# Performance work log

Hardware: AMD Instinct MI355X
Metric: run time of the kernel (lower is better)

The kernel has to match this reference:

```python
import jax, jax.numpy as jnp
import numpy as np

N = 5000      # batch entities / prompts
M = 50000     # flattened neighbors
R = 500000    # flattened (neighbor, relation) pairs
D = 768
VOCAB = 10000


def setup_inputs() -> dict:
    key = jax.random.key(0)
    ks = jax.random.split(key, 12)
    start_emb = jax.random.normal(ks[0], (N, D), dtype=jnp.float32)
    prompt_emb = jax.random.normal(ks[1], (N, D), dtype=jnp.float32)
    relation_emb = jax.random.normal(ks[2], (R, D), dtype=jnp.float32)
    neighbor_emb = jax.random.normal(ks[3], (M, D), dtype=jnp.float32)
    count_table = jax.random.normal(ks[4], (VOCAB, D), dtype=jnp.float32) * 0.02
    W = jax.random.normal(ks[5], (1, 4 * D), dtype=jnp.float32) * 0.02
    b = jnp.zeros((1,), dtype=jnp.float32)
    counts = jax.random.randint(ks[6], (R,), 0, VOCAB)
    rel_start_idx = jax.random.randint(ks[7], (R,), 0, N)
    neighbor_idx = jnp.sort(jax.random.randint(ks[8], (R,), 0, M))
    start_idx = jax.random.randint(ks[9], (M,), 0, N)
    return {
        "start_emb": start_emb, "prompt_emb": prompt_emb,
        "relation_emb": relation_emb, "neighbor_emb": neighbor_emb,
        "count_table": count_table, "W": W, "b": b,
        "counts": counts, "rel_start_idx": rel_start_idx,
        "neighbor_idx": neighbor_idx, "start_idx": start_idx,
    }


def _segment_softmax(logits, seg, num_segments):
    # numerically stable softmax within each neighbor segment
    seg_max = jax.ops.segment_max(logits, seg, num_segments=num_segments)
    ex = jnp.exp(logits - seg_max[seg])
    denom = jax.ops.segment_sum(ex, seg, num_segments=num_segments)
    return ex / denom[seg]


def reference(start_emb, prompt_emb, relation_emb, neighbor_emb,
              count_table, W, b,
              counts, rel_start_idx, neighbor_idx, start_idx):
    num_neighbors = neighbor_emb.shape[0]
    # relation_emb = relation_emb * count_embs(counts)   [R, D]
    rel = relation_emb * count_table[counts]
    # per-relation logit: <start_emb[rel_start_idx], rel>  [R]
    s_rel = start_emb[rel_start_idx]
    logits = jnp.sum(s_rel * rel, axis=1)
    # scatter_softmax over neighbor segments, then scatter_add aggregation
    alpha = _segment_softmax(logits, neighbor_idx, num_neighbors)
    rel_agg = jax.ops.segment_sum(rel * alpha[:, None], neighbor_idx,
                                  num_segments=num_neighbors)  # [M, D]
    # gather per-neighbor start / prompt embeddings
    s_n = start_emb[start_idx]      # [M, D]
    p_n = prompt_emb[start_idx]     # [M, D]
    # AttentionScorer: concat then Linear(4D -> 1), squeeze
    combined = jnp.concatenate([s_n, p_n, rel_agg, neighbor_emb], axis=1)
    score = (combined @ W.T + b).squeeze(-1)  # [M]
    return score
```

## Files before the change

kernel.cpp:

```cpp
#include <hip/hip_runtime.h>
#include <math.h>

#define WAVE 64

__device__ inline float wave_reduce_sum(float v) {
    #pragma unroll
    for (int off = 32; off > 0; off >>= 1)
        v += __shfl_xor(v, off, WAVE);
    return v;
}

__device__ inline unsigned int f32_to_e4m3(float a) {
    unsigned int u = __float_as_uint(a);
    unsigned int sgn = (u >> 31) << 7;
    unsigned int absu = u & 0x7FFFFFFFu;
    if (absu < 0x3C800000u) return sgn;
    int exp = (int)(absu >> 23) - 127;
    unsigned int m = absu & 0x7FFFFFu;
    unsigned int keep = m >> 20;
    unsigned int rest = m & 0xFFFFFu;
    if (rest > 0x80000u || (rest == 0x80000u && (keep & 1u))) keep++;
    if (keep == 8u) { keep = 0u; exp += 1; }
    if (exp > 8) { exp = 8; keep = 7u; }
    return sgn | ((unsigned int)(exp + 7) << 3) | keep;
}

__device__ inline float e4m3_to_f32(unsigned int b) {
    unsigned int expm = b & 0x7Fu;
    unsigned int f = ((b & 0x80u) << 24) | ((expm + (120u << 3)) << 20);
    float v = __uint_as_float(f);
    return (expm & 0x78u) ? v : 0.0f;
}

__device__ inline void decode4_fp8(unsigned int u, float& a, float& b, float& c, float& d) {
#if __has_builtin(__builtin_amdgcn_cvt_pk_f32_fp8)
    auto lo = __builtin_amdgcn_cvt_pk_f32_fp8(u, false);
    auto hi = __builtin_amdgcn_cvt_pk_f32_fp8(u, true);
    a = lo[0]; b = lo[1]; c = hi[0]; d = hi[1];
#else
    a = e4m3_to_f32(u & 0xFFu);
    b = e4m3_to_f32((u >> 8) & 0xFFu);
    c = e4m3_to_f32((u >> 16) & 0xFFu);
    d = e4m3_to_f32((u >> 24) & 0xFFu);
#endif
}

__global__ void cvt_fp8_kernel(const float* __restrict__ in,
                               unsigned int* __restrict__ out,
                               int n4, float scale) {
    int i = blockIdx.x * blockDim.x + threadIdx.x;
    if (i >= n4) return;
    float4 v = ((const float4*)in)[i];
    unsigned int b0 = f32_to_e4m3(v.x * scale);
    unsigned int b1 = f32_to_e4m3(v.y * scale);
    unsigned int b2 = f32_to_e4m3(v.z * scale);
    unsigned int b3 = f32_to_e4m3(v.w * scale);
    out[i] = b0 | (b1 << 8) | (b2 << 16) | (b3 << 24);
}

__global__ void entity_dots_kernel(const float* __restrict__ start_emb,
                                   const float* __restrict__ prompt_emb,
                                   const float* __restrict__ W,
                                   float* __restrict__ ew, int N, int D) {
    int wavesPerBlock = blockDim.x >> 6;
    int i = blockIdx.x * wavesPerBlock + (threadIdx.x >> 6);
    int lane = threadIdx.x & 63;
    if (i >= N) return;
    const float* s  = start_emb  + (size_t)i * D;
    const float* p  = prompt_emb + (size_t)i * D;
    const float* w0 = W;
    const float* w1 = W + D;
    float acc = 0.f;
    for (int idx = lane * 4; idx < D; idx += WAVE * 4) {
        float4 sv  = *(const float4*)(s  + idx);
        float4 pv  = *(const float4*)(p  + idx);
        float4 w0v = *(const float4*)(w0 + idx);
        float4 w1v = *(const float4*)(w1 + idx);
        acc = fmaf(sv.x, w0v.x, acc);
        acc = fmaf(sv.y, w0v.y, acc);
        acc = fmaf(sv.z, w0v.z, acc);
        acc = fmaf(sv.w, w0v.w, acc);
        acc = fmaf(pv.x, w1v.x, acc);
        acc = fmaf(pv.y, w1v.y, acc);
        acc = fmaf(pv.z, w1v.z, acc);
        acc = fmaf(pv.w, w1v.w, acc);
    }
    acc = wave_reduce_sum(acc);
    if (lane == 0) ew[i] = acc;
}

template <int DD>
__global__ __launch_bounds__(256) void relation_kernel2_t(
        const float* __restrict__ relation_emb,
        const unsigned char* __restrict__ ctf8,
        const unsigned char* __restrict__ sf8,
        const float* __restrict__ W,
        const int* __restrict__ counts,
        const int* __restrict__ rel_start_idx,
        float2* __restrict__ lt,
        int R, float inv_ct_scale) {
    int w = blockIdx.x * (blockDim.x >> 6) + (threadIdx.x >> 6);
    int lane = threadIdx.x & 63;
    int r0 = w << 1;
    if (r0 >= R) return;
    bool has2 = (r0 + 1 < R);

    int cnt0 = counts[r0];
    int st0  = rel_start_idx[r0];
    int cnt1 = has2 ? counts[r0 + 1] : cnt0;
    int st1  = has2 ? rel_start_idx[r0 + 1] : st0;

    const float* re0 = relation_emb + (size_t)r0 * DD;
    const float* re1 = re0 + (has2 ? DD : 0);
    const unsigned int* ct0 = (const unsigned int*)(ctf8 + (size_t)cnt0 * DD);
    const unsigned int* ct1 = (const unsigned int*)(ctf8 + (size_t)cnt1 * DD);
    const unsigned int* se0 = (const unsigned int*)(sf8 + (size_t)st0 * DD);
    const unsigned int* se1 = (const unsigned int*)(sf8 + (size_t)st1 * DD);
    const float* w2 = W + 2 * (size_t)DD;

    float lg0 = 0.f, tt0 = 0.f, lg1 = 0.f, tt1 = 0.f;
    #pragma unroll
    for (int idx = 0; idx < DD; idx += WAVE * 4) {
        int e4 = idx + lane * 4;
        int e1 = (idx >> 2) + lane;
        float4 rv0 = *(const float4*)(re0 + e4);
        float4 rv1 = *(const float4*)(re1 + e4);
        float4 wv  = *(const float4*)(w2 + e4);
        unsigned int cu0 = ct0[e1], su0 = se0[e1];
        unsigned int cu1 = ct1[e1], su1 = se1[e1];
        {
            float c0,c1,c2,c3, s0,s1,s2,s3;
            decode4_fp8(cu0, c0,c1,c2,c3);
            decode4_fp8(su0, s0,s1,s2,s3);
            float x0 = rv0.x*c0, x1 = rv0.y*c1, x2 = rv0.z*c2, x3 = rv0.w*c3;
            lg0 = fmaf(s0,x0, fmaf(s1,x1, fmaf(s2,x2, fmaf(s3,x3, lg0))));
            tt0 = fmaf(wv.x,x0, fmaf(wv.y,x1, fmaf(wv.z,x2, fmaf(wv.w,x3, tt0))));
        }
        {
            float c0,c1,c2,c3, s0,s1,s2,s3;
            decode4_fp8(cu1, c0,c1,c2,c3);
            decode4_fp8(su1, s0,s1,s2,s3);
            float x0 = rv1.x*c0, x1 = rv1.y*c1, x2 = rv1.z*c2, x3 = rv1.w*c3;
            lg1 = fmaf(s0,x0, fmaf(s1,x1, fmaf(s2,x2, fmaf(s3,x3, lg1))));
            tt1 = fmaf(wv.x,x0, fmaf(wv.y,x1, fmaf(wv.z,x2, fmaf(wv.w,x3, tt1))));
        }
    }
    lg0 = wave_reduce_sum(lg0) * inv_ct_scale;
    tt0 = wave_reduce_sum(tt0) * inv_ct_scale;
    lg1 = wave_reduce_sum(lg1) * inv_ct_scale;
    tt1 = wave_reduce_sum(tt1) * inv_ct_scale;
    if (lane == 0) {
        if (has2) {
            float4 v; v.x = lg0; v.y = tt0; v.z = lg1; v.w = tt1;
            *(float4*)(lt + r0) = v;
        } else {
            lt[r0] = make_float2(lg0, tt0);
        }
    }
}

__global__ void relation_kernel_gen(const float* __restrict__ relation_emb,
                                    const unsigned char* __restrict__ ctf8,
                                    const unsigned char* __restrict__ sf8,
                                    const float* __restrict__ W,
                                    const int* __restrict__ counts,
                                    const int* __restrict__ rel_start_idx,
                                    float2* __restrict__ lt,
                                    int R, int D, float inv_ct_scale) {
    int r = blockIdx.x * (blockDim.x >> 6) + (threadIdx.x >> 6);
    int lane = threadIdx.x & 63;
    if (r >= R) return;
    const float* re = relation_emb + (size_t)r * D;
    const unsigned int* ct = (const unsigned int*)(ctf8 + (size_t)counts[r] * D);
    const unsigned int* se = (const unsigned int*)(sf8 + (size_t)rel_start_idx[r] * D);
    const float* w2 = W + 2 * (size_t)D;
    float lg = 0.f, tt = 0.f;
    for (int idx = lane * 4; idx < D; idx += WAVE * 4) {
        float4 rv = *(const float4*)(re + idx);
        float4 wv = *(const float4*)(w2 + idx);
        float c0,c1,c2,c3, s0,s1,s2,s3;
        decode4_fp8(ct[idx >> 2], c0,c1,c2,c3);
        decode4_fp8(se[idx >> 2], s0,s1,s2,s3);
        float x0 = rv.x*c0, x1 = rv.y*c1, x2 = rv.z*c2, x3 = rv.w*c3;
        lg = fmaf(s0,x0, fmaf(s1,x1, fmaf(s2,x2, fmaf(s3,x3, lg))));
        tt = fmaf(wv.x,x0, fmaf(wv.y,x1, fmaf(wv.z,x2, fmaf(wv.w,x3, tt))));
    }
    lg = wave_reduce_sum(lg) * inv_ct_scale;
    tt = wave_reduce_sum(tt) * inv_ct_scale;
    if (lane == 0) lt[r] = make_float2(lg, tt);
}

__global__ void seg_init_kernel(int* __restrict__ segs, int* __restrict__ sege, int M) {
    int m = blockIdx.x * blockDim.x + threadIdx.x;
    if (m < M) { segs[m] = 0; sege[m] = 0; }
}

__global__ void seg_mark_kernel(const int* __restrict__ neighbor_idx,
                                int* __restrict__ segs, int* __restrict__ sege, int R) {
    int r = blockIdx.x * blockDim.x + threadIdx.x;
    if (r >= R) return;
    int cur = neighbor_idx[r];
    if (r == 0) {
        segs[cur] = 0;
    } else {
        int prev = neighbor_idx[r - 1];
        if (prev != cur) {
            segs[cur] = r;
            sege[prev] = r;
        }
    }
    if (r == R - 1) sege[cur] = R;
}

__global__ void segment_kernel(const float2* __restrict__ lt,
                               const int* __restrict__ segs,
                               const int* __restrict__ sege,
                               float* __restrict__ c,
                               int M) {
    int m = blockIdx.x * blockDim.x + threadIdx.x;
    if (m >= M) return;
    int s = segs[m], e = sege[m];
    if (e <= s) { c[m] = 0.f; return; }
    float mx = -INFINITY;
    for (int i = s; i < e; ++i) mx = fmaxf(mx, lt[i].x);
    float den = 0.f, num = 0.f;
    for (int i = s; i < e; ++i) {
        float2 v = lt[i];
        float ex = expf(v.x - mx);
        den += ex;
        num = fmaf(ex, v.y, num);
    }
    c[m] = num / den;
}

__global__ void score_kernel(const float* __restrict__ neighbor_emb,
                             const float* __restrict__ W,
                             const float* __restrict__ bptr,
                             const int* __restrict__ start_idx,
                             const float* __restrict__ ew,
                             const float* __restrict__ c,
                             float* __restrict__ out,
                             int M, int D) {
    int wavesPerBlock = blockDim.x >> 6;
    int m = blockIdx.x * wavesPerBlock + (threadIdx.x >> 6);
    int lane = threadIdx.x & 63;
    if (m >= M) return;
    const float* nb = neighbor_emb + (size_t)m * D;
    const float* w3 = W + 3 * (size_t)D;
    float acc = 0.f;
    for (int idx = lane * 4; idx < D; idx += WAVE * 4) {
        float4 nv = *(const float4*)(nb + idx);
        float4 wv = *(const float4*)(w3 + idx);
        acc = fmaf(nv.x, wv.x, acc);
        acc = fmaf(nv.y, wv.y, acc);
        acc = fmaf(nv.z, wv.z, acc);
        acc = fmaf(nv.w, wv.w, acc);
    }
    acc = wave_reduce_sum(acc);
    if (lane == 0) {
        out[m] = acc + ew[start_idx[m]] + c[m] + bptr[0];
    }
}

extern "C" void kernel_launch(void* const* d_in, const int* in_sizes, int n_in,
                              void* d_out, int out_size, void* d_ws, size_t ws_size,
                              hipStream_t stream) {
    const float* start_emb    = (const float*)d_in[0];
    const float* prompt_emb   = (const float*)d_in[1];
    const float* relation_emb = (const float*)d_in[2];
    const float* neighbor_emb = (const float*)d_in[3];
    const float* count_table  = (const float*)d_in[4];
    const float* W            = (const float*)d_in[5];
    const float* b            = (const float*)d_in[6];
    const int*   counts        = (const int*)d_in[7];
    const int*   rel_start_idx = (const int*)d_in[8];
    const int*   neighbor_idx  = (const int*)d_in[9];
    const int*   start_idx     = (const int*)d_in[10];

    int D = in_sizes[5] / 4;
    int N = in_sizes[0] / D;
    int R = in_sizes[7];
    int M = in_sizes[10];
    int VOCAB = in_sizes[4] / D;

    const float CT_SCALE = 64.0f;

    char* ws = (char*)d_ws;
    size_t off = 0;
    float*  ew   = (float*)(ws + off);  off += ((size_t)N * 4 + 255) & ~(size_t)255;
    float2* lt   = (float2*)(ws + off); off += ((size_t)R * 8 + 255) & ~(size_t)255;
    float*  c    = (float*)(ws + off);  off += ((size_t)M * 4 + 255) & ~(size_t)255;
    int*    segs = (int*)(ws + off);    off += ((size_t)M * 4 + 255) & ~(size_t)255;
    int*    sege = (int*)(ws + off);    off += ((size_t)M * 4 + 255) & ~(size_t)255;
    unsigned char* ctf8 = (unsigned char*)(ws + off); off += ((size_t)VOCAB * D + 255) & ~(size_t)255;
    unsigned char* sf8  = (unsigned char*)(ws + off); off += ((size_t)N * D + 255) & ~(size_t)255;
    float*  out  = (float*)d_out;

    {
        int n4 = (VOCAB * D) / 4;
        cvt_fp8_kernel<<<(n4 + 255) / 256, 256, 0, stream>>>(count_table,
                                                             (unsigned int*)ctf8, n4, CT_SCALE);
        int m4 = (N * D) / 4;
        cvt_fp8_kernel<<<(m4 + 255) / 256, 256, 0, stream>>>(start_emb,
                                                             (unsigned int*)sf8, m4, 1.0f);
    }
    seg_init_kernel<<<(M + 255) / 256, 256, 0, stream>>>(segs, sege, M);
    seg_mark_kernel<<<(R + 255) / 256, 256, 0, stream>>>(neighbor_idx, segs, sege, R);

    {
        int grid = (N + 3) / 4;
        entity_dots_kernel<<<grid, 256, 0, stream>>>(start_emb, prompt_emb, W, ew, N, D);
    }
    {
        if (D == 768) {
            int nw = (R + 1) / 2;
            int grid = (nw + 3) / 4;
            relation_kernel2_t<768><<<grid, 256, 0, stream>>>(
                relation_emb, ctf8, sf8, W, counts, rel_start_idx, lt, R, 1.0f / CT_SCALE);
        } else {
            int grid = (R + 3) / 4;
            relation_kernel_gen<<<grid, 256, 0, stream>>>(
                relation_emb, ctf8, sf8, W, counts, rel_start_idx, lt, R, D, 1.0f / CT_SCALE);
        }
    }
    {
        int grid = (M + 255) / 256;
        segment_kernel<<<grid, 256, 0, stream>>>(lt, segs, sege, c, M);
    }
    {
        int grid = (M + 3) / 4;
        score_kernel<<<grid, 256, 0, stream>>>(neighbor_emb, W, b, start_idx, ew, c, out, M, D);
    }
}
```

Baseline: 363.3 us.

## Process relations in count-sorted order via counting sort permutation

Builds a permutation of relations sorted by their count index (histogram, single-block scan, atomic scatter) and has the relation kernel process relations in that order. Relations sharing the same count_table row then run close together, which is meant to improve cache reuse of the fp8 count-table rows. In exchange, relation_emb rows are read in a scattered order instead of streaming sequentially, lt writes become scattered, and four extra small kernels are launched, including a serial one-block scan.

```diff
diff --git a/kernel.cpp b/kernel.cpp
--- a/kernel.cpp
+++ b/kernel.cpp
@@ -89,29 +89,79 @@
     if (lane == 0) ew[i] = acc;
 }
 
+__global__ void init_kernel(int* __restrict__ segs, int* __restrict__ sege,
+                            int* __restrict__ hist, int M, int V) {
+    int i = blockIdx.x * blockDim.x + threadIdx.x;
+    if (i < M) { segs[i] = 0; sege[i] = 0; }
+    if (i < V) hist[i] = 0;
+}
+
+__global__ void hist_kernel(const int* __restrict__ counts,
+                            int* __restrict__ hist, int R) {
+    int r = blockIdx.x * blockDim.x + threadIdx.x;
+    if (r < R) atomicAdd(&hist[counts[r]], 1);
+}
+
+__global__ __launch_bounds__(1024) void scan_kernel(const int* __restrict__ hist,
+                                                    int* __restrict__ binpos, int V) {
+    __shared__ int partial[1024];
+    int t = threadIdx.x;
+    int per = (V + 1023) / 1024;
+    int base = t * per;
+    int lim = base + per; if (lim > V) lim = V;
+    int sum = 0;
+    for (int i = base; i < lim; ++i) sum += hist[i];
+    partial[t] = sum;
+    __syncthreads();
+    for (int ofs = 1; ofs < 1024; ofs <<= 1) {
+        int v = (t >= ofs) ? partial[t - ofs] : 0;
+        __syncthreads();
+        partial[t] += v;
+        __syncthreads();
+    }
+    int run = (t == 0) ? 0 : partial[t - 1];
+    for (int i = base; i < lim; ++i) {
+        binpos[i] = run;
+        run += hist[i];
+    }
+}
+
+__global__ void scatter_kernel(const int* __restrict__ counts,
+                               int* __restrict__ binpos,
+                               int* __restrict__ perm, int R) {
+    int r = blockIdx.x * blockDim.x + threadIdx.x;
+    if (r >= R) return;
+    int pos = atomicAdd(&binpos[counts[r]], 1);
+    perm[pos] = r;
+}
+
 template <int DD>
-__global__ __launch_bounds__(256) void relation_kernel2_t(
+__global__ __launch_bounds__(256) void relation_kernel2_sorted_t(
         const float* __restrict__ relation_emb,
         const unsigned char* __restrict__ ctf8,
         const unsigned char* __restrict__ sf8,
         const float* __restrict__ W,
         const int* __restrict__ counts,
         const int* __restrict__ rel_start_idx,
+        const int* __restrict__ perm,
         float2* __restrict__ lt,
         int R, float inv_ct_scale) {
     int w = blockIdx.x * (blockDim.x >> 6) + (threadIdx.x >> 6);
     int lane = threadIdx.x & 63;
-    int r0 = w << 1;
-    if (r0 >= R) return;
-    bool has2 = (r0 + 1 < R);
+    int p0 = w << 1;
+    if (p0 >= R) return;
+    bool has2 = (p0 + 1 < R);
+
+    int r0 = perm[p0];
+    int r1 = has2 ? perm[p0 + 1] : r0;
 
     int cnt0 = counts[r0];
     int st0  = rel_start_idx[r0];
-    int cnt1 = has2 ? counts[r0 + 1] : cnt0;
-    int st1  = has2 ? rel_start_idx[r0 + 1] : st0;
+    int cnt1 = counts[r1];
+    int st1  = rel_start_idx[r1];
 
     const float* re0 = relation_emb + (size_t)r0 * DD;
-    const float* re1 = re0 + (has2 ? DD : 0);
+    const float* re1 = relation_emb + (size_t)r1 * DD;
     const unsigned int* ct0 = (const unsigned int*)(ctf8 + (size_t)cnt0 * DD);
     const unsigned int* ct1 = (const unsigned int*)(ctf8 + (size_t)cnt1 * DD);
     const unsigned int* se0 = (const unsigned int*)(sf8 + (size_t)st0 * DD);
@@ -150,12 +200,8 @@
     lg1 = wave_reduce_sum(lg1) * inv_ct_scale;
     tt1 = wave_reduce_sum(tt1) * inv_ct_scale;
     if (lane == 0) {
-        if (has2) {
-            float4 v; v.x = lg0; v.y = tt0; v.z = lg1; v.w = tt1;
-            *(float4*)(lt + r0) = v;
-        } else {
-            lt[r0] = make_float2(lg0, tt0);
-        }
+        lt[r0] = make_float2(lg0, tt0);
+        if (has2) lt[r1] = make_float2(lg1, tt1);
     }
 }
 
@@ -190,11 +236,6 @@
     if (lane == 0) lt[r] = make_float2(lg, tt);
 }
 
-__global__ void seg_init_kernel(int* __restrict__ segs, int* __restrict__ sege, int M) {
-    int m = blockIdx.x * blockDim.x + threadIdx.x;
-    if (m < M) { segs[m] = 0; sege[m] = 0; }
-}
-
 __global__ void seg_mark_kernel(const int* __restrict__ neighbor_idx,
                                 int* __restrict__ segs, int* __restrict__ sege, int R) {
     int r = blockIdx.x * blockDim.x + threadIdx.x;
@@ -292,6 +333,9 @@
     float*  c    = (float*)(ws + off);  off += ((size_t)M * 4 + 255) & ~(size_t)255;
     int*    segs = (int*)(ws + off);    off += ((size_t)M * 4 + 255) & ~(size_t)255;
     int*    sege = (int*)(ws + off);    off += ((size_t)M * 4 + 255) & ~(size_t)255;
+    int*    hist = (int*)(ws + off);    off += ((size_t)VOCAB * 4 + 255) & ~(size_t)255;
+    int*    binpos = (int*)(ws + off);  off += ((size_t)VOCAB * 4 + 255) & ~(size_t)255;
+    int*    perm = (int*)(ws + off);    off += ((size_t)R * 4 + 255) & ~(size_t)255;
     unsigned char* ctf8 = (unsigned char*)(ws + off); off += ((size_t)VOCAB * D + 255) & ~(size_t)255;
     unsigned char* sf8  = (unsigned char*)(ws + off); off += ((size_t)N * D + 255) & ~(size_t)255;
     float*  out  = (float*)d_out;
@@ -304,9 +348,14 @@
         cvt_fp8_kernel<<<(m4 + 255) / 256, 256, 0, stream>>>(start_emb,
                                                              (unsigned int*)sf8, m4, 1.0f);
     }
-    seg_init_kernel<<<(M + 255) / 256, 256, 0, stream>>>(segs, sege, M);
-    seg_mark_kernel<<<(R + 255) / 256, 256, 0, stream>>>(neighbor_idx, segs, sege, R);
-
+    {
+        int mx = M > VOCAB ? M : VOCAB;
+        init_kernel<<<(mx + 255) / 256, 256, 0, stream>>>(segs, sege, hist, M, VOCAB);
+        seg_mark_kernel<<<(R + 255) / 256, 256, 0, stream>>>(neighbor_idx, segs, sege, R);
+        hist_kernel<<<(R + 255) / 256, 256, 0, stream>>>(counts, hist, R);
+        scan_kernel<<<1, 1024, 0, stream>>>(hist, binpos, VOCAB);
+        scatter_kernel<<<(R + 255) / 256, 256, 0, stream>>>(counts, binpos, perm, R);
+    }
     {
         int grid = (N + 3) / 4;
         entity_dots_kernel<<<grid, 256, 0, stream>>>(start_emb, prompt_emb, W, ew, N, D);
@@ -315,8 +364,8 @@
         if (D == 768) {
             int nw = (R + 1) / 2;
             int grid = (nw + 3) / 4;
-            relation_kernel2_t<768><<<grid, 256, 0, stream>>>(
-                relation_emb, ctf8, sf8, W, counts, rel_start_idx, lt, R, 1.0f / CT_SCALE);
+            relation_kernel2_sorted_t<768><<<grid, 256, 0, stream>>>(
+                relation_emb, ctf8, sf8, W, counts, rel_start_idx, perm, lt, R, 1.0f / CT_SCALE);
         } else {
             int grid = (R + 3) / 4;
             relation_kernel_gen<<<grid, 256, 0, stream>>>(
```

New measurement: 479.2 us. +31.9%, slower.
